# Kernel tuning notes

Measured on AMD Instinct MI355X. Metric: run time of the kernel, lower is better.

The kernel has to match this reference:

```python
import jax, jax.numpy as jnp
import numpy as np

TEMPERATURE = 0.5
F_EPS = 1e-12   # torch F.normalize default eps
COS_EPS = 1e-8  # torch cosine_similarity default eps


def setup_inputs() -> dict:
    key = jax.random.key(0)
    k1, k2, k3 = jax.random.split(key, 3)
    B, S, D, T = 64, 2048, 256, 64
    features = jax.random.normal(k1, (B, S, D), dtype=jnp.float32)
    labels = jax.random.randint(k2, (B, S), 0, T)
    label_emb = jax.random.normal(k3, (T, D), dtype=jnp.float32)  # nn.Embedding weight
    return {"features": features, "labels": labels, "label_emb": label_emb}


def reference(features, labels, label_emb):
    # features: [B, S, D], labels: [B, S] int, label_emb: [T, D]
    num_tags = label_emb.shape[0]
    mask = jax.nn.one_hot(labels, num_tags, dtype=features.dtype)  # [B, S, T]

    # F.normalize(features, p=2, dim=-1): x / max(||x||, eps)
    f = features / jnp.maximum(
        jnp.linalg.norm(features, axis=-1, keepdims=True), F_EPS)
    # cosine_similarity(proto, f): f already unit-norm, so only proto norm matters
    p = label_emb / jnp.maximum(
        jnp.linalg.norm(label_emb, axis=-1, keepdims=True), COS_EPS)

    # nested-loop get_att_dis == one batched matmul of unit vectors
    sim = jnp.einsum('bsd,td->bst', f, p)  # [B, S, T] cosine similarities

    inv_t = 1.0 / TEMPERATURE
    pos = jnp.sum(jnp.exp(sim * mask * inv_t) * mask, axis=-1)          # [B, S]
    neg_mask = 1.0 - mask
    neg = jnp.sum(jnp.exp(sim * neg_mask * inv_t) * neg_mask, axis=-1)  # [B, S]

    loss = -jnp.log(pos / neg)
    return loss.sum()
```

## Files before the change

kernel.cpp:

```cpp
#include <hip/hip_runtime.h>
#include <math.h>

typedef __attribute__((ext_vector_type(8))) short bf16x8;
typedef __attribute__((ext_vector_type(4))) float f32x4;

#define NTAGS 64

__device__ __forceinline__ short f2bf(float f) {
    unsigned u = __builtin_bit_cast(unsigned, f);
    u += 0x7fffu + ((u >> 16) & 1u);
    return (short)(u >> 16);
}

__global__ __launch_bounds__(256)
void lcl_prep(const float* __restrict__ lemb, bf16x8* __restrict__ ws)
{
    __shared__ float part[4][NTAGS];
    __shared__ float scl[NTAGS];
    const int tid = threadIdx.x;
    const float4* lemb4 = (const float4*)lemb;
    {
        int t = tid & 63, p = tid >> 6;
        float ss = 0.f;
        #pragma unroll
        for (int j = 0; j < 16; ++j) {
            float4 q = lemb4[t * 64 + p * 16 + j];
            ss += q.x*q.x + q.y*q.y + q.z*q.z + q.w*q.w;
        }
        part[p][t] = ss;
    }
    __syncthreads();
    if (tid < NTAGS) {
        float ss = part[0][tid] + part[1][tid] + part[2][tid] + part[3][tid];
        scl[tid] = 1.0f / fmaxf(sqrtf(ss), 1e-8f);
    }
    __syncthreads();
    const int e = blockIdx.x * 256 + tid;
    const int chunk = e >> 6, t = e & 63;
    const float s = scl[t];
    float4 q0 = lemb4[t * 64 + chunk * 2];
    float4 q1 = lemb4[t * 64 + chunk * 2 + 1];
    bf16x8 pk;
    pk[0] = f2bf(q0.x * s); pk[1] = f2bf(q0.y * s);
    pk[2] = f2bf(q0.z * s); pk[3] = f2bf(q0.w * s);
    pk[4] = f2bf(q1.x * s); pk[5] = f2bf(q1.y * s);
    pk[6] = f2bf(q1.z * s); pk[7] = f2bf(q1.w * s);
    ws[e] = pk;
}

__global__ __launch_bounds__(512, 4)
void lcl_main(const float* __restrict__ feat,
              const int*   __restrict__ labels,
              const bf16x8* __restrict__ protoWS,
              float*       __restrict__ blockPart)
{
    __shared__ bf16x8 protoB[2048];
    __shared__ float  wsum[8];
    const int tid  = threadIdx.x;
    const int lane = tid & 63;
    const int wv   = tid >> 6;
    const int g = lane >> 4;
    const int r = lane & 15;
    const int r0 = (blockIdx.x * 8 + wv) * 16;
    const float4* feat4 = (const float4*)feat;

    bf16x8 pw[4];
    #pragma unroll
    for (int i = 0; i < 4; ++i) pw[i] = protoWS[i * 512 + tid];

    const size_t base = (size_t)(r0 + r) * 64 + g * 2;
    float4 q[16];
    #pragma unroll
    for (int ks = 0; ks < 8; ++ks) {
        q[2 * ks]     = feat4[base + ks * 8];
        q[2 * ks + 1] = feat4[base + ks * 8 + 1];
    }
    const int4 lb = ((const int4*)labels)[(r0 >> 2) + g];

    #pragma unroll
    for (int i = 0; i < 4; ++i) protoB[i * 512 + tid] = pw[i];

    #pragma unroll
    for (int i = 0; i < 16; ++i)
        asm volatile("" :: "v"(q[i].x), "v"(q[i].y), "v"(q[i].z), "v"(q[i].w));
    __syncthreads();

    f32x4 acc[4];
    #pragma unroll
    for (int ct = 0; ct < 4; ++ct) acc[ct] = (f32x4){0.f, 0.f, 0.f, 0.f};

    float sqa = 0.f, sqb = 0.f;
    #pragma unroll
    for (int ks = 0; ks < 8; ++ks) {
        float4 q0 = q[2 * ks], q1 = q[2 * ks + 1];
        sqa = fmaf(q0.x, q0.x, fmaf(q0.y, q0.y, fmaf(q0.z, q0.z, fmaf(q0.w, q0.w, sqa))));
        sqb = fmaf(q1.x, q1.x, fmaf(q1.y, q1.y, fmaf(q1.z, q1.z, fmaf(q1.w, q1.w, sqb))));
        bf16x8 af;
        af[0] = f2bf(q0.x); af[1] = f2bf(q0.y);
        af[2] = f2bf(q0.z); af[3] = f2bf(q0.w);
        af[4] = f2bf(q1.x); af[5] = f2bf(q1.y);
        af[6] = f2bf(q1.z); af[7] = f2bf(q1.w);
        const int cbase = (ks * 4 + g) * 64;
        #pragma unroll
        for (int ct = 0; ct < 4; ++ct)
            acc[ct] = __builtin_amdgcn_mfma_f32_16x16x32_bf16(
                          af, protoB[cbase + ct * 16 + r], acc[ct], 0, 0, 0);
    }

    float sq = sqa + sqb;
    sq += __shfl_xor(sq, 16, 64);
    sq += __shfl_xor(sq, 32, 64);
    const float rn = 1.0f / fmaxf(sqrtf(sq), 1e-12f);

    float wloss = 0.f;
    #pragma unroll
    for (int reg = 0; reg < 4; ++reg) {
        const int rowi = g * 4 + reg;
        float rr  = __shfl(rn, rowi, 64);
        const int lbl = (reg == 0) ? lb.x : (reg == 1) ? lb.y : (reg == 2) ? lb.z : lb.w;
        float en = 0.f, pos = 0.f;
        #pragma unroll
        for (int ct = 0; ct < 4; ++ct) {
            float sim = acc[ct][reg] * rr;
            float e   = __expf(2.0f * sim);
            bool  m   = (lbl == ct * 16 + r);
            en  += m ? 0.f : e;
            pos += m ? 2.0f * sim : 0.f;
        }
        #pragma unroll
        for (int o = 1; o < 16; o <<= 1) {
            en  += __shfl_xor(en,  o, 64);
            pos += __shfl_xor(pos, o, 64);
        }
        wloss += __logf(en) - pos;
    }

    wloss += __shfl_xor(wloss, 16, 64);
    wloss += __shfl_xor(wloss, 32, 64);
    if (lane == 0) wsum[wv] = wloss;
    __syncthreads();
    if (tid == 0) {
        blockPart[blockIdx.x] = wsum[0] + wsum[1] + wsum[2] + wsum[3]
                              + wsum[4] + wsum[5] + wsum[6] + wsum[7];
    }
}

__global__ __launch_bounds__(256)
void lcl_reduce(const float* __restrict__ part, float* __restrict__ out)
{
    __shared__ float s[4];
    const int tid = threadIdx.x;
    float v = part[tid] + part[tid + 256] + part[tid + 512] + part[tid + 768];
    #pragma unroll
    for (int o = 1; o < 64; o <<= 1) v += __shfl_xor(v, o, 64);
    if ((tid & 63) == 0) s[tid >> 6] = v;
    __syncthreads();
    if (tid == 0) out[0] = s[0] + s[1] + s[2] + s[3];
}

extern "C" void kernel_launch(void* const* d_in, const int* in_sizes, int n_in,
                              void* d_out, int out_size, void* d_ws, size_t ws_size,
                              hipStream_t stream) {
    const float* feat   = (const float*)d_in[0];
    const int*   labels = (const int*)d_in[1];
    const float* lemb   = (const float*)d_in[2];
    float*       out    = (float*)d_out;
    bf16x8*      ws     = (bf16x8*)d_ws;
    float*       part   = (float*)((char*)d_ws + 32768);

    lcl_prep<<<8, 256, 0, stream>>>(lemb, ws);

    const int nrows = in_sizes[1];
    const int grid  = nrows / (8 * 16);
    lcl_main<<<grid, 512, 0, stream>>>(feat, labels, ws, part);
    lcl_reduce<<<1, 256, 0, stream>>>(part, out);
}
```

Baseline: 34.82 us.

## Fuse prototype normalization into main kernel and raise occupancy hint

Removes the separate prep kernel that normalized and bf16-packed the label embeddings. Each main-kernel block now computes the prototype norms itself and writes the packed prototypes straight into shared memory. This saves one kernel launch and its dependency, at the cost of redundant per-block work (64KB of embedding reads plus extra barriers) in every block. The launch-bounds minimum-blocks hint goes from 4 to 8, and the empty asm register pin on the feature loads is dropped.

New measurement: 57.16 us. 64.2% more time.

```diff
diff --git a/kernel.cpp b/kernel.cpp
--- a/kernel.cpp
+++ b/kernel.cpp
@@ -12,49 +12,15 @@
     return (short)(u >> 16);
 }
 
-__global__ __launch_bounds__(256)
-void lcl_prep(const float* __restrict__ lemb, bf16x8* __restrict__ ws)
-{
-    __shared__ float part[4][NTAGS];
-    __shared__ float scl[NTAGS];
-    const int tid = threadIdx.x;
-    const float4* lemb4 = (const float4*)lemb;
-    {
-        int t = tid & 63, p = tid >> 6;
-        float ss = 0.f;
-        #pragma unroll
-        for (int j = 0; j < 16; ++j) {
-            float4 q = lemb4[t * 64 + p * 16 + j];
-            ss += q.x*q.x + q.y*q.y + q.z*q.z + q.w*q.w;
-        }
-        part[p][t] = ss;
-    }
-    __syncthreads();
-    if (tid < NTAGS) {
-        float ss = part[0][tid] + part[1][tid] + part[2][tid] + part[3][tid];
-        scl[tid] = 1.0f / fmaxf(sqrtf(ss), 1e-8f);
-    }
-    __syncthreads();
-    const int e = blockIdx.x * 256 + tid;
-    const int chunk = e >> 6, t = e & 63;
-    const float s = scl[t];
-    float4 q0 = lemb4[t * 64 + chunk * 2];
-    float4 q1 = lemb4[t * 64 + chunk * 2 + 1];
-    bf16x8 pk;
-    pk[0] = f2bf(q0.x * s); pk[1] = f2bf(q0.y * s);
-    pk[2] = f2bf(q0.z * s); pk[3] = f2bf(q0.w * s);
-    pk[4] = f2bf(q1.x * s); pk[5] = f2bf(q1.y * s);
-    pk[6] = f2bf(q1.z * s); pk[7] = f2bf(q1.w * s);
-    ws[e] = pk;
-}
-
-__global__ __launch_bounds__(512, 4)
+__global__ __launch_bounds__(512, 8)
 void lcl_main(const float* __restrict__ feat,
               const int*   __restrict__ labels,
-              const bf16x8* __restrict__ protoWS,
+              const float* __restrict__ lemb,
               float*       __restrict__ blockPart)
 {
     __shared__ bf16x8 protoB[2048];
+    __shared__ float  part[8][NTAGS];
+    __shared__ float  scl[NTAGS];
     __shared__ float  wsum[8];
     const int tid  = threadIdx.x;
     const int lane = tid & 63;
@@ -63,10 +29,7 @@
     const int r = lane & 15;
     const int r0 = (blockIdx.x * 8 + wv) * 16;
     const float4* feat4 = (const float4*)feat;
-
-    bf16x8 pw[4];
-    #pragma unroll
-    for (int i = 0; i < 4; ++i) pw[i] = protoWS[i * 512 + tid];
+    const float4* lemb4 = (const float4*)lemb;
 
     const size_t base = (size_t)(r0 + r) * 64 + g * 2;
     float4 q[16];
@@ -77,12 +40,37 @@
     }
     const int4 lb = ((const int4*)labels)[(r0 >> 2) + g];
 
+    {
+        int t = tid & 63, p = tid >> 6;
+        float ss = 0.f;
+        #pragma unroll
+        for (int j = 0; j < 8; ++j) {
+            float4 qq = lemb4[t * 64 + p * 8 + j];
+            ss += qq.x*qq.x + qq.y*qq.y + qq.z*qq.z + qq.w*qq.w;
+        }
+        part[p][t] = ss;
+    }
+    __syncthreads();
+    if (tid < NTAGS) {
+        float ss = part[0][tid] + part[1][tid] + part[2][tid] + part[3][tid]
+                 + part[4][tid] + part[5][tid] + part[6][tid] + part[7][tid];
+        scl[tid] = 1.0f / fmaxf(sqrtf(ss), 1e-8f);
+    }
+    __syncthreads();
     #pragma unroll
-    for (int i = 0; i < 4; ++i) protoB[i * 512 + tid] = pw[i];
-
-    #pragma unroll
-    for (int i = 0; i < 16; ++i)
-        asm volatile("" :: "v"(q[i].x), "v"(q[i].y), "v"(q[i].z), "v"(q[i].w));
+    for (int i = 0; i < 4; ++i) {
+        int e = i * 512 + tid;
+        int chunk = e >> 6, t = e & 63;
+        float s = scl[t];
+        float4 q0 = lemb4[t * 64 + chunk * 2];
+        float4 q1 = lemb4[t * 64 + chunk * 2 + 1];
+        bf16x8 pk;
+        pk[0] = f2bf(q0.x * s); pk[1] = f2bf(q0.y * s);
+        pk[2] = f2bf(q0.z * s); pk[3] = f2bf(q0.w * s);
+        pk[4] = f2bf(q1.x * s); pk[5] = f2bf(q1.y * s);
+        pk[6] = f2bf(q1.z * s); pk[7] = f2bf(q1.w * s);
+        protoB[e] = pk;
+    }
     __syncthreads();
 
     f32x4 acc[4];
@@ -165,13 +153,10 @@
     const int*   labels = (const int*)d_in[1];
     const float* lemb   = (const float*)d_in[2];
     float*       out    = (float*)d_out;
-    bf16x8*      ws     = (bf16x8*)d_ws;
-    float*       part   = (float*)((char*)d_ws + 32768);
-
-    lcl_prep<<<8, 256, 0, stream>>>(lemb, ws);
+    float*       bpart  = (float*)d_ws;
 
     const int nrows = in_sizes[1];
     const int grid  = nrows / (8 * 16);
-    lcl_main<<<grid, 512, 0, stream>>>(feat, labels, ws, part);
-    lcl_reduce<<<1, 256, 0, stream>>>(part, out);
+    lcl_main<<<grid, 512, 0, stream>>>(feat, labels, lemb, bpart);
+    lcl_reduce<<<1, 256, 0, stream>>>(bpart, out);
 }
```
